# Performance work log

Measured on AMD Instinct MI355X. Metric: run time of the kernel, lower is better.

Reference implementation:

```python
import jax, jax.numpy as jnp
import numpy as np

ROPE_THETA = 10000.0

def _apply_rope(t):
    # t: [B, H, S, D]; rotate interleaved even/odd pairs
    B, H, S, D = t.shape
    inv_freq = 1.0 / (ROPE_THETA ** (jnp.arange(0, D, 2, dtype=jnp.float32) / D))  # [D/2]
    ang = jnp.arange(S, dtype=jnp.float32)[:, None] * inv_freq[None, :]            # [S, D/2]
    cos = jnp.cos(ang)[None, None]  # [1,1,S,D/2]
    sin = jnp.sin(ang)[None, None]
    te = t[..., 0::2]
    to = t[..., 1::2]
    re = te * cos - to * sin
    ro = te * sin + to * cos
    out = jnp.stack([re, ro], axis=-1).reshape(B, H, S, D)
    return out

def setup_inputs() -> dict:
    key = jax.random.key(0)
    ks = jax.random.split(key, 5)
    B, S, DIM = 2, 2048, 2048
    x = jax.random.normal(ks[0], (B, S, DIM), dtype=jnp.float32)
    scale = 0.02
    Wq = jax.random.normal(ks[1], (DIM, DIM), dtype=jnp.float32) * scale
    Wk = jax.random.normal(ks[2], (DIM, DIM), dtype=jnp.float32) * scale
    Wv = jax.random.normal(ks[3], (DIM, DIM), dtype=jnp.float32) * scale
    Wo = jax.random.normal(ks[4], (DIM, DIM), dtype=jnp.float32) * scale
    return {"x": x, "Wq": Wq, "Wk": Wk, "Wv": Wv, "Wo": Wo}

def reference(x, Wq, Wk, Wv, Wo):
    B, S, DIM = x.shape
    H = 16
    HD = DIM // H
    # nn.Linear(bias=False) with weight [out,in]: y = x @ W.T; here W stored [in,out]
    q = (x @ Wq).reshape(B, S, H, HD).transpose(0, 2, 1, 3)  # [B,H,S,HD]
    k = (x @ Wk).reshape(B, S, H, HD).transpose(0, 2, 1, 3)
    v = (x @ Wv).reshape(B, S, H, HD).transpose(0, 2, 1, 3)
    q = _apply_rope(q)
    k = _apply_rope(k)
    scores = jnp.einsum('bhqd,bhkd->bhqk', q, k) / jnp.sqrt(jnp.float32(HD))  # [B,H,S,S]
    causal = jnp.tril(jnp.ones((S, S), dtype=bool))
    scores = jnp.where(causal[None, None], scores, jnp.float32(-jnp.inf))
    attn = jax.nn.softmax(scores, axis=-1)
    out = jnp.einsum('bhqk,bhkd->bhqd', attn, v)            # [B,H,S,HD]
    out = out.transpose(0, 2, 1, 3).reshape(B, S, DIM)
    return out @ Wo  # output projection (dropout is identity in eval)
```

## Files before the change

kernel.cpp:

```cpp
#include <hip/hip_runtime.h>
#include <hip/hip_bf16.h>
#include <math.h>

typedef __bf16 bf16;
typedef __attribute__((ext_vector_type(2))) __bf16 bf16x2;
typedef __attribute__((ext_vector_type(4))) __bf16 bf16x4;
typedef __attribute__((ext_vector_type(8))) __bf16 bf16x8;
typedef __attribute__((ext_vector_type(4))) float f32x4;

#define LDS_ASYNC16(gptr, lptr)                                                        \
  __builtin_amdgcn_global_load_lds(                                                    \
      (const __attribute__((address_space(1))) void*)(gptr),                           \
      (__attribute__((address_space(3))) void*)(lptr), 16, 0, 0)

constexpr int BATCH = 2, SEQ = 2048, DIM = 2048, NH = 16, HD = 128;
constexpr float QSC = 0.12751744f;
constexpr float FREQC = 0.20762050593046f;

template <int CTRL>
__device__ __forceinline__ float dpp_mov_f(float x) {
  return __int_as_float(__builtin_amdgcn_update_dpp(
      __float_as_int(x), __float_as_int(x), CTRL, 0xf, 0xf, false));
}
__device__ __forceinline__ float rowmax16(float x) {
  x = fmaxf(x, dpp_mov_f<0x121>(x));
  x = fmaxf(x, dpp_mov_f<0x122>(x));
  x = fmaxf(x, dpp_mov_f<0x124>(x));
  x = fmaxf(x, dpp_mov_f<0x128>(x));
  return x;
}
__device__ __forceinline__ float rowsum16(float x) {
  x += dpp_mov_f<0x121>(x);
  x += dpp_mov_f<0x122>(x);
  x += dpp_mov_f<0x124>(x);
  x += dpp_mov_f<0x128>(x);
  return x;
}

__global__ void cvt_f32_to_bf16(const float4* __restrict__ in,
                                bf16x4* __restrict__ out, int n4) {
  int i = blockIdx.x * blockDim.x + threadIdx.x;
  if (i >= n4) return;
  float4 v = in[i];
  bf16x4 o;
  o[0] = (bf16)v.x; o[1] = (bf16)v.y; o[2] = (bf16)v.z; o[3] = (bf16)v.w;
  out[i] = o;
}

__global__ void transpose_w4(const float* __restrict__ W0, const float* __restrict__ W1,
                             const float* __restrict__ W2, const float* __restrict__ W3,
                             bf16* __restrict__ T0, bf16* __restrict__ T3) {
  __shared__ float tile[32][33];
  const int z = blockIdx.z;
  const float* W = (z == 0) ? W0 : (z == 1) ? W1 : (z == 2) ? W2 : W3;
  bf16* WT = (z == 3) ? T3 : (T0 + (size_t)z * DIM * DIM);
  int tx = threadIdx.x, ty = threadIdx.y;
  int bx = blockIdx.x * 32, by = blockIdx.y * 32;
#pragma unroll
  for (int j = 0; j < 32; j += 8)
    tile[ty + j][tx] = W[(size_t)(by + ty + j) * DIM + bx + tx];
  __syncthreads();
#pragma unroll
  for (int j = 0; j < 32; j += 8)
    WT[(size_t)(bx + ty + j) * DIM + by + tx] = (bf16)tile[tx][ty + j];
}

__device__ __forceinline__ int swz_src(int c) {
  return (c & 3) ^ ((c >> 3) & 3);
}
__device__ __forceinline__ int swz_rd(int quad, int ln) {
  return quad ^ ((ln >> 1) & 3);
}

__global__ __launch_bounds__(256) void gemm_qkv(const bf16* __restrict__ A,
                                                const bf16* __restrict__ BT,
                                                bf16* __restrict__ Qb,
                                                bf16* __restrict__ Kb,
                                                bf16* __restrict__ VTo) {
  __shared__ __attribute__((aligned(16))) bf16 As[128 * 32];
  __shared__ __attribute__((aligned(16))) bf16 Bs[128 * 32];
  const int tid = threadIdx.x;
  const int w = tid >> 6, lane = tid & 63;
  const int quad = lane >> 4, ln = lane & 15;
  const int m0 = blockIdx.y * 128, n0 = blockIdx.x * 128;
  const int wm = (w >> 1) * 64, wn = (w & 1) * 64;
  const int rdc = swz_rd(quad, ln) * 8;
  f32x4 acc[4][4] = {};

  for (int k0 = 0; k0 < DIM; k0 += 32) {
#pragma unroll
    for (int i = 0; i < 2; ++i) {
      const int c = i * 256 + tid;
      LDS_ASYNC16(A  + (size_t)(m0 + (c >> 2)) * DIM + k0 + swz_src(c) * 8,
                  As + (size_t)(i * 256 + w * 64) * 8);
      LDS_ASYNC16(BT + (size_t)(n0 + (c >> 2)) * DIM + k0 + swz_src(c) * 8,
                  Bs + (size_t)(i * 256 + w * 64) * 8);
    }
    __syncthreads();
    bf16x8 af[4], bfr[4];
#pragma unroll
    for (int t = 0; t < 4; ++t)
      af[t] = *(const bf16x8*)(As + (wm + t * 16 + ln) * 32 + rdc);
#pragma unroll
    for (int t = 0; t < 4; ++t)
      bfr[t] = *(const bf16x8*)(Bs + (wn + t * 16 + ln) * 32 + rdc);
#pragma unroll
    for (int mt = 0; mt < 4; ++mt)
#pragma unroll
      for (int nt = 0; nt < 4; ++nt)
        acc[mt][nt] = __builtin_amdgcn_mfma_f32_16x16x32_bf16(
            af[mt], bfr[nt], acc[mt][nt], 0, 0, 0);
    __syncthreads();
  }

  const int sel = n0 >> 11;
  if (sel == 2) {
#pragma unroll
    for (int mt = 0; mt < 4; ++mt)
#pragma unroll
      for (int nt = 0; nt < 4; ++nt) {
        int gr = m0 + wm + mt * 16 + quad * 4;
        int fc = (n0 + wn + nt * 16 + ln) & 2047;
        int b = gr >> 11, s0 = gr & (SEQ - 1);
        int h = fc >> 7, d = fc & (HD - 1);
        bf16x4 pk;
#pragma unroll
        for (int r = 0; r < 4; ++r) pk[r] = (bf16)acc[mt][nt][r];
        *(bf16x4*)(VTo + ((size_t)((b * NH + h) * HD + d)) * SEQ + s0) = pk;
      }
  } else {
    bf16* Dst = sel ? Kb : Qb;
    const float osc = sel ? 1.0f : QSC;
#pragma unroll
    for (int nt = 0; nt < 4; ++nt) {
      int gc = n0 + wn + nt * 16 + ln;
      int fc = gc & 2047, d = fc & (HD - 1);
      float freq = exp2f(-(float)(d >> 1) * FREQC);
      bool ev = !(d & 1);
#pragma unroll
      for (int mt = 0; mt < 4; ++mt) {
#pragma unroll
        for (int r = 0; r < 4; ++r) {
          int gr = m0 + wm + mt * 16 + quad * 4 + r;
          int s = gr & (SEQ - 1);
          float ang = (float)s * freq;
          float sn, cs;
          __sincosf(ang, &sn, &cs);
          float own = acc[mt][nt][r];
          float oth = __shfl_xor(own, 1);
          float res = ev ? (own * cs - oth * sn) : (oth * sn + own * cs);
          Dst[(size_t)gr * DIM + fc] = (bf16)(res * osc);
        }
      }
    }
  }
}

template <int MODE>
__global__ __launch_bounds__(256) void gemm_bt(const bf16* __restrict__ A,
                                               const bf16* __restrict__ BT,
                                               void* __restrict__ C) {
  __shared__ __attribute__((aligned(16))) bf16 As[128 * 32];
  __shared__ __attribute__((aligned(16))) bf16 Bs[128 * 32];
  const int tid = threadIdx.x;
  const int w = tid >> 6, lane = tid & 63;
  const int quad = lane >> 4, ln = lane & 15;
  const int m0 = blockIdx.y * 128, n0 = blockIdx.x * 128;
  const int wm = (w >> 1) * 64, wn = (w & 1) * 64;
  const int rdc = swz_rd(quad, ln) * 8;
  f32x4 acc[4][4] = {};

  for (int k0 = 0; k0 < DIM; k0 += 32) {
#pragma unroll
    for (int i = 0; i < 2; ++i) {
      const int c = i * 256 + tid;
      LDS_ASYNC16(A  + (size_t)(m0 + (c >> 2)) * DIM + k0 + swz_src(c) * 8,
                  As + (size_t)(i * 256 + w * 64) * 8);
      LDS_ASYNC16(BT + (size_t)(n0 + (c >> 2)) * DIM + k0 + swz_src(c) * 8,
                  Bs + (size_t)(i * 256 + w * 64) * 8);
    }
    __syncthreads();
    bf16x8 af[4], bfr[4];
#pragma unroll
    for (int t = 0; t < 4; ++t)
      af[t] = *(const bf16x8*)(As + (wm + t * 16 + ln) * 32 + rdc);
#pragma unroll
    for (int t = 0; t < 4; ++t)
      bfr[t] = *(const bf16x8*)(Bs + (wn + t * 16 + ln) * 32 + rdc);
#pragma unroll
    for (int mt = 0; mt < 4; ++mt)
#pragma unroll
      for (int nt = 0; nt < 4; ++nt)
        acc[mt][nt] = __builtin_amdgcn_mfma_f32_16x16x32_bf16(
            af[mt], bfr[nt], acc[mt][nt], 0, 0, 0);
    __syncthreads();
  }

  if (MODE == 0) {
    bf16* Co = (bf16*)C;
#pragma unroll
    for (int mt = 0; mt < 4; ++mt)
#pragma unroll
      for (int nt = 0; nt < 4; ++nt) {
        int gr = m0 + wm + mt * 16 + quad * 4;
        int gc = n0 + wn + nt * 16 + ln;
#pragma unroll
        for (int r = 0; r < 4; ++r)
          Co[(size_t)(gr + r) * DIM + gc] = (bf16)acc[mt][nt][r];
      }
  } else {
    float* Co = (float*)C;
#pragma unroll
    for (int mt = 0; mt < 4; ++mt)
#pragma unroll
      for (int nt = 0; nt < 4; ++nt) {
        int gr = m0 + wm + mt * 16 + quad * 4;
        int gc = n0 + wn + nt * 16 + ln;
#pragma unroll
        for (int r = 0; r < 4; ++r)
          Co[(size_t)(gr + r) * DIM + gc] = acc[mt][nt][r];
      }
  }
}

constexpr int PSTR = 72;
__global__ __launch_bounds__(256, 3) void flash_attn(
    const bf16* __restrict__ Q, const bf16* __restrict__ K,
    const bf16* __restrict__ VT, bf16* __restrict__ O,
    bf16* __restrict__ Opart, float* __restrict__ Mpart,
    float* __restrict__ Lpart) {
  __shared__ __attribute__((aligned(16))) bf16 Ks[64 * 128];
  __shared__ __attribute__((aligned(16))) bf16 VTs[128 * 64];
  __shared__ __attribute__((aligned(16))) bf16 Ps[4][32 * PSTR];
  const int tid = threadIdx.x;
  const int w = tid >> 6, lane = tid & 63, quad = lane >> 4, ln = lane & 15;
  const int e = blockIdx.x;
  const int t = (e < 8) ? e : (8 + ((e - 8) >> 1));
  const int c0 = (e < 8) ? 0 : ((e - 8) & 1);
  const bool partial = (e >= 8);
  const int q0 = t * 128;
  const int ktN = 2 * (t + 1);
  const int kt0 = c0 * 16;
  const int kt1 = partial ? ((c0 == 0) ? 16 : ktN) : ktN;
  const int b = blockIdx.y >> 4, h = blockIdx.y & 15;

  bf16x8 qf[2][4];
#pragma unroll
  for (int mt = 0; mt < 2; ++mt)
#pragma unroll
    for (int kc = 0; kc < 4; ++kc)
      qf[mt][kc] = *(const bf16x8*)(Q + ((size_t)b * SEQ + q0 + w * 32 + mt * 16 + ln) * DIM +
                                    h * HD + kc * 32 + quad * 8);
  f32x4 o[2][8] = {};
  float mst[2][4], lst[2][4];
#pragma unroll
  for (int mt = 0; mt < 2; ++mt)
#pragma unroll
    for (int r = 0; r < 4; ++r) { mst[mt][r] = -1e30f; lst[mt][r] = 0.f; }

  for (int kt = kt0; kt < kt1; ++kt) {
    __syncthreads();
#pragma unroll
    for (int i = 0; i < 4; ++i) {
      const int c = i * 256 + tid;
      LDS_ASYNC16(K + ((size_t)b * SEQ + kt * 64 + (c >> 4)) * DIM + h * HD +
                      (((c & 15) ^ ((c >> 4) & 15)) * 8),
                  Ks + (size_t)(i * 256 + w * 64) * 8);
      LDS_ASYNC16(VT + ((size_t)((b * NH + h) * HD) + (c >> 3)) * SEQ + kt * 64 +
                      (((c & 7) ^ ((c >> 3) & 7)) * 8),
                  VTs + (size_t)(i * 256 + w * 64) * 8);
    }
    __syncthreads();

    f32x4 s[2][4] = {};
#pragma unroll
    for (int nt = 0; nt < 4; ++nt) {
      bf16x8 kf[4];
#pragma unroll
      for (int kc = 0; kc < 4; ++kc)
        kf[kc] = *(const bf16x8*)(Ks + (nt * 16 + ln) * 128 +
                                  (((kc * 4 + quad) ^ ln) * 8));
#pragma unroll
      for (int kc = 0; kc < 4; ++kc)
#pragma unroll
        for (int mt = 0; mt < 2; ++mt)
          s[mt][nt] = __builtin_amdgcn_mfma_f32_16x16x32_bf16(
              qf[mt][kc], kf[kc], s[mt][nt], 0, 0, 0);
    }

    const bool diag = (kt * 64 + 63 > q0);
    if (diag) {
#pragma unroll
      for (int mt = 0; mt < 2; ++mt)
#pragma unroll
        for (int nt = 0; nt < 4; ++nt)
#pragma unroll
          for (int r = 0; r < 4; ++r) {
            int kg = kt * 64 + nt * 16 + ln;
            int qg = q0 + w * 32 + mt * 16 + quad * 4 + r;
            if (kg > qg) s[mt][nt][r] = -1e30f;
          }
    }

#pragma unroll
    for (int mt = 0; mt < 2; ++mt)
#pragma unroll
      for (int r = 0; r < 4; ++r) {
        float rm = fmaxf(fmaxf(s[mt][0][r], s[mt][1][r]),
                         fmaxf(s[mt][2][r], s[mt][3][r]));
        rm = rowmax16(rm);
        float mold = mst[mt][r];
        float mnew = fmaxf(mold, rm);
        float alpha = exp2f(mold - mnew);
        mst[mt][r] = mnew;
        float rs = 0.f;
#pragma unroll
        for (int nt = 0; nt < 4; ++nt) {
          float p = exp2f(s[mt][nt][r] - mnew);
          rs += p;
          Ps[w][(mt * 16 + quad * 4 + r) * PSTR + nt * 16 + ln] = (bf16)p;
        }
        lst[mt][r] = lst[mt][r] * alpha + rs;
#pragma unroll
        for (int nd = 0; nd < 8; ++nd) o[mt][nd][r] *= alpha;
      }
    __syncthreads();

#pragma unroll
    for (int kc2 = 0; kc2 < 2; ++kc2) {
      bf16x8 pf[2];
#pragma unroll
      for (int mt = 0; mt < 2; ++mt)
        pf[mt] = *(const bf16x8*)(&Ps[w][(mt * 16 + ln) * PSTR + kc2 * 32 + quad * 8]);
#pragma unroll
      for (int nd = 0; nd < 8; ++nd) {
        bf16x8 vf = *(const bf16x8*)(VTs + (nd * 16 + ln) * 64 +
                                     (((kc2 * 4 + quad) ^ (ln & 7)) * 8));
#pragma unroll
        for (int mt = 0; mt < 2; ++mt)
          o[mt][nd] = __builtin_amdgcn_mfma_f32_16x16x32_bf16(
              pf[mt], vf, o[mt][nd], 0, 0, 0);
      }
    }
  }

  if (!partial) {
#pragma unroll
    for (int mt = 0; mt < 2; ++mt)
#pragma unroll
      for (int r = 0; r < 4; ++r) {
        float inv = 1.f / rowsum16(lst[mt][r]);
        int qg = q0 + w * 32 + mt * 16 + quad * 4 + r;
#pragma unroll
        for (int nd = 0; nd < 8; ++nd)
          O[((size_t)b * SEQ + qg) * DIM + h * HD + nd * 16 + ln] =
              (bf16)(o[mt][nd][r] * inv);
      }
  } else {
    const int slot = (((blockIdx.y << 3) + (t - 8)) << 1) + c0;
    bf16* Op = Opart + (size_t)slot * (128 * 128);
#pragma unroll
    for (int mt = 0; mt < 2; ++mt)
#pragma unroll
      for (int r = 0; r < 4; ++r) {
        float l = rowsum16(lst[mt][r]);
        int qr = w * 32 + mt * 16 + quad * 4 + r;
        if (ln == 0) {
          Mpart[slot * 128 + qr] = mst[mt][r];
          Lpart[slot * 128 + qr] = l;
        }
#pragma unroll
        for (int nd = 0; nd < 8; ++nd)
          Op[qr * 128 + nd * 16 + ln] = (bf16)o[mt][nd][r];
      }
  }
}

__global__ __launch_bounds__(256) void flash_merge(const bf16* __restrict__ Opart,
                                                   const float* __restrict__ Mpart,
                                                   const float* __restrict__ Lpart,
                                                   bf16* __restrict__ O) {
  const int g = blockIdx.x;
  const int bh = g >> 3, t = 8 + (g & 7);
  const int b = bh >> 4, h = bh & 15;
  const int row = threadIdx.x >> 1, half = threadIdx.x & 1;
  const int s0 = g * 2, s1 = g * 2 + 1;
  float m0 = Mpart[s0 * 128 + row], m1 = Mpart[s1 * 128 + row];
  float l0 = Lpart[s0 * 128 + row], l1 = Lpart[s1 * 128 + row];
  float M = fmaxf(m0, m1);
  float w0 = exp2f(m0 - M), w1 = exp2f(m1 - M);
  float inv = 1.f / (w0 * l0 + w1 * l1);
  w0 *= inv; w1 *= inv;
  const bf16* p0 = Opart + (size_t)s0 * (128 * 128) + row * 128 + half * 64;
  const bf16* p1 = Opart + (size_t)s1 * (128 * 128) + row * 128 + half * 64;
  bf16* dst = O + ((size_t)b * SEQ + t * 128 + row) * DIM + h * HD + half * 64;
#pragma unroll
  for (int j = 0; j < 8; ++j) {
    bf16x8 a = *(const bf16x8*)(p0 + j * 8);
    bf16x8 c = *(const bf16x8*)(p1 + j * 8);
    bf16x8 o8;
#pragma unroll
    for (int k = 0; k < 8; ++k)
      o8[k] = (bf16)(w0 * (float)a[k] + w1 * (float)c[k]);
    *(bf16x8*)(dst + j * 8) = o8;
  }
}

extern "C" void kernel_launch(void* const* d_in, const int* in_sizes, int n_in,
                              void* d_out, int out_size, void* d_ws, size_t ws_size,
                              hipStream_t stream) {
  (void)in_sizes; (void)n_in; (void)out_size; (void)ws_size;
  const float* x  = (const float*)d_in[0];
  const float* Wq = (const float*)d_in[1];
  const float* Wk = (const float*)d_in[2];
  const float* Wv = (const float*)d_in[3];
  const float* Wo = (const float*)d_in[4];

  char* ws = (char*)d_ws;
  const size_t MB = 1u << 20;
  const size_t WB = (size_t)DIM * DIM * 2;
  bf16* WTqkv = (bf16*)(ws);
  bf16* WoT   = (bf16*)(ws + 3 * WB);
  bf16* xb    = (bf16*)(ws + 32 * MB);
  bf16* Qb    = (bf16*)(ws + 48 * MB);
  bf16* Kb    = (bf16*)(ws + 64 * MB);
  bf16* VT    = (bf16*)(ws + 80 * MB);
  bf16* Ab    = xb;
  bf16*  Opart = (bf16*)(ws);
  float* Mpart = (float*)(ws + 16 * MB);
  float* Lpart = (float*)(ws + 16 * MB + 256 * 1024);

  int n4 = BATCH * SEQ * DIM / 4;
  cvt_f32_to_bf16<<<n4 / 256, 256, 0, stream>>>((const float4*)x, (bf16x4*)xb, n4);
  dim3 tb(32, 8), tg(DIM / 32, DIM / 32, 4);
  transpose_w4<<<tg, tb, 0, stream>>>(Wq, Wk, Wv, Wo, WTqkv, WoT);

  dim3 qg(3 * DIM / 128, BATCH * SEQ / 128);
  gemm_qkv<<<qg, 256, 0, stream>>>(xb, WTqkv, Qb, Kb, VT);

  dim3 fg(24, BATCH * NH);
  flash_attn<<<fg, 256, 0, stream>>>(Qb, Kb, VT, Ab, Opart, Mpart, Lpart);
  flash_merge<<<256, 256, 0, stream>>>(Opart, Mpart, Lpart, Ab);

  dim3 gg(DIM / 128, BATCH * SEQ / 128);
  gemm_bt<2><<<gg, 256, 0, stream>>>(Ab, WoT, d_out);
}
```

Measured before the change: 469.4 us.

## Double GEMM K-tile to 64 with XOR swizzle and rebalance flash-attention split-K chunks

Both bf16 GEMMs now stage 64-wide K tiles in LDS with an 8-way XOR swizzle, so each barrier pair covers two MFMA k-steps. This halves the number of syncs and load rounds per GEMM, at the cost of twice the LDS per block. Flash attention now splits causal query tiles into chunks of at most 10 key tiles (1 to 4 chunks per tile, 34 blocks per head) instead of a fixed split of the last 8 tiles. The first chunk writes straight into the output buffer, and the merge kernel combines up to 4 partials in place. This aims to balance work across blocks and reduce the tail, in exchange for more partial traffic and more complex indexing.

```diff
diff --git a/kernel.cpp b/kernel.cpp
--- a/kernel.cpp
+++ b/kernel.cpp
@@ -65,51 +65,51 @@
     WT[(size_t)(bx + ty + j) * DIM + by + tx] = (bf16)tile[tx][ty + j];
 }
 
-__device__ __forceinline__ int swz_src(int c) {
-  return (c & 3) ^ ((c >> 3) & 3);
-}
-__device__ __forceinline__ int swz_rd(int quad, int ln) {
-  return quad ^ ((ln >> 1) & 3);
-}
 
 __global__ __launch_bounds__(256) void gemm_qkv(const bf16* __restrict__ A,
                                                 const bf16* __restrict__ BT,
                                                 bf16* __restrict__ Qb,
                                                 bf16* __restrict__ Kb,
                                                 bf16* __restrict__ VTo) {
-  __shared__ __attribute__((aligned(16))) bf16 As[128 * 32];
-  __shared__ __attribute__((aligned(16))) bf16 Bs[128 * 32];
+  __shared__ __attribute__((aligned(16))) bf16 As[128 * 64];
+  __shared__ __attribute__((aligned(16))) bf16 Bs[128 * 64];
   const int tid = threadIdx.x;
   const int w = tid >> 6, lane = tid & 63;
   const int quad = lane >> 4, ln = lane & 15;
   const int m0 = blockIdx.y * 128, n0 = blockIdx.x * 128;
   const int wm = (w >> 1) * 64, wn = (w & 1) * 64;
-  const int rdc = swz_rd(quad, ln) * 8;
+  const int l7 = ln & 7;
   f32x4 acc[4][4] = {};
 
-  for (int k0 = 0; k0 < DIM; k0 += 32) {
-#pragma unroll
-    for (int i = 0; i < 2; ++i) {
+  for (int k0 = 0; k0 < DIM; k0 += 64) {
+#pragma unroll
+    for (int i = 0; i < 4; ++i) {
       const int c = i * 256 + tid;
-      LDS_ASYNC16(A  + (size_t)(m0 + (c >> 2)) * DIM + k0 + swz_src(c) * 8,
+      const int row = c >> 3, p = c & 7;
+      LDS_ASYNC16(A  + (size_t)(m0 + row) * DIM + k0 + ((p ^ (row & 7)) * 8),
                   As + (size_t)(i * 256 + w * 64) * 8);
-      LDS_ASYNC16(BT + (size_t)(n0 + (c >> 2)) * DIM + k0 + swz_src(c) * 8,
+      LDS_ASYNC16(BT + (size_t)(n0 + row) * DIM + k0 + ((p ^ (row & 7)) * 8),
                   Bs + (size_t)(i * 256 + w * 64) * 8);
     }
     __syncthreads();
-    bf16x8 af[4], bfr[4];
-#pragma unroll
-    for (int t = 0; t < 4; ++t)
-      af[t] = *(const bf16x8*)(As + (wm + t * 16 + ln) * 32 + rdc);
-#pragma unroll
-    for (int t = 0; t < 4; ++t)
-      bfr[t] = *(const bf16x8*)(Bs + (wn + t * 16 + ln) * 32 + rdc);
-#pragma unroll
-    for (int mt = 0; mt < 4; ++mt)
-#pragma unroll
-      for (int nt = 0; nt < 4; ++nt)
-        acc[mt][nt] = __builtin_amdgcn_mfma_f32_16x16x32_bf16(
-            af[mt], bfr[nt], acc[mt][nt], 0, 0, 0);
+#pragma unroll
+    for (int kh = 0; kh < 2; ++kh) {
+      bf16x8 af[4], bfr[4];
+#pragma unroll
+      for (int t = 0; t < 4; ++t)
+        af[t] = *(const bf16x8*)(As + (wm + t * 16 + ln) * 64 +
+                                 (((kh * 4 + quad) ^ l7) * 8));
+#pragma unroll
+      for (int t = 0; t < 4; ++t)
+        bfr[t] = *(const bf16x8*)(Bs + (wn + t * 16 + ln) * 64 +
+                                  (((kh * 4 + quad) ^ l7) * 8));
+#pragma unroll
+      for (int mt = 0; mt < 4; ++mt)
+#pragma unroll
+        for (int nt = 0; nt < 4; ++nt)
+          acc[mt][nt] = __builtin_amdgcn_mfma_f32_16x16x32_bf16(
+              af[mt], bfr[nt], acc[mt][nt], 0, 0, 0);
+    }
     __syncthreads();
   }
 
@@ -160,39 +160,45 @@
 __global__ __launch_bounds__(256) void gemm_bt(const bf16* __restrict__ A,
                                                const bf16* __restrict__ BT,
                                                void* __restrict__ C) {
-  __shared__ __attribute__((aligned(16))) bf16 As[128 * 32];
-  __shared__ __attribute__((aligned(16))) bf16 Bs[128 * 32];
+  __shared__ __attribute__((aligned(16))) bf16 As[128 * 64];
+  __shared__ __attribute__((aligned(16))) bf16 Bs[128 * 64];
   const int tid = threadIdx.x;
   const int w = tid >> 6, lane = tid & 63;
   const int quad = lane >> 4, ln = lane & 15;
   const int m0 = blockIdx.y * 128, n0 = blockIdx.x * 128;
   const int wm = (w >> 1) * 64, wn = (w & 1) * 64;
-  const int rdc = swz_rd(quad, ln) * 8;
+  const int l7 = ln & 7;
   f32x4 acc[4][4] = {};
 
-  for (int k0 = 0; k0 < DIM; k0 += 32) {
-#pragma unroll
-    for (int i = 0; i < 2; ++i) {
+  for (int k0 = 0; k0 < DIM; k0 += 64) {
+#pragma unroll
+    for (int i = 0; i < 4; ++i) {
       const int c = i * 256 + tid;
-      LDS_ASYNC16(A  + (size_t)(m0 + (c >> 2)) * DIM + k0 + swz_src(c) * 8,
+      const int row = c >> 3, p = c & 7;
+      LDS_ASYNC16(A  + (size_t)(m0 + row) * DIM + k0 + ((p ^ (row & 7)) * 8),
                   As + (size_t)(i * 256 + w * 64) * 8);
-      LDS_ASYNC16(BT + (size_t)(n0 + (c >> 2)) * DIM + k0 + swz_src(c) * 8,
+      LDS_ASYNC16(BT + (size_t)(n0 + row) * DIM + k0 + ((p ^ (row & 7)) * 8),
                   Bs + (size_t)(i * 256 + w * 64) * 8);
     }
     __syncthreads();
-    bf16x8 af[4], bfr[4];
-#pragma unroll
-    for (int t = 0; t < 4; ++t)
-      af[t] = *(const bf16x8*)(As + (wm + t * 16 + ln) * 32 + rdc);
-#pragma unroll
-    for (int t = 0; t < 4; ++t)
-      bfr[t] = *(const bf16x8*)(Bs + (wn + t * 16 + ln) * 32 + rdc);
-#pragma unroll
-    for (int mt = 0; mt < 4; ++mt)
-#pragma unroll
-      for (int nt = 0; nt < 4; ++nt)
-        acc[mt][nt] = __builtin_amdgcn_mfma_f32_16x16x32_bf16(
-            af[mt], bfr[nt], acc[mt][nt], 0, 0, 0);
+#pragma unroll
+    for (int kh = 0; kh < 2; ++kh) {
+      bf16x8 af[4], bfr[4];
+#pragma unroll
+      for (int t = 0; t < 4; ++t)
+        af[t] = *(const bf16x8*)(As + (wm + t * 16 + ln) * 64 +
+                                 (((kh * 4 + quad) ^ l7) * 8));
+#pragma unroll
+      for (int t = 0; t < 4; ++t)
+        bfr[t] = *(const bf16x8*)(Bs + (wn + t * 16 + ln) * 64 +
+                                  (((kh * 4 + quad) ^ l7) * 8));
+#pragma unroll
+      for (int mt = 0; mt < 4; ++mt)
+#pragma unroll
+        for (int nt = 0; nt < 4; ++nt)
+          acc[mt][nt] = __builtin_amdgcn_mfma_f32_16x16x32_bf16(
+              af[mt], bfr[nt], acc[mt][nt], 0, 0, 0);
+    }
     __syncthreads();
   }
 
@@ -221,6 +227,13 @@
           Co[(size_t)(gr + r) * DIM + gc] = acc[mt][nt][r];
       }
   }
+}
+
+__device__ __forceinline__ int ml_off(int t) {
+  return (t < 10) ? 2 * (t - 5) : (t < 15) ? 10 + 3 * (t - 10) : 25;
+}
+__device__ __forceinline__ int op_off(int t) {
+  return (t < 10) ? (t - 5) : (t < 15) ? 5 + 2 * (t - 10) : 15;
 }
 
 constexpr int PSTR = 72;
@@ -235,14 +248,18 @@
   const int tid = threadIdx.x;
   const int w = tid >> 6, lane = tid & 63, quad = lane >> 4, ln = lane & 15;
   const int e = blockIdx.x;
-  const int t = (e < 8) ? e : (8 + ((e - 8) >> 1));
-  const int c0 = (e < 8) ? 0 : ((e - 8) & 1);
-  const bool partial = (e >= 8);
+  int t, c0, nc;
+  if (e < 5)       { t = e;                  c0 = 0;               nc = 1; }
+  else if (e < 15) { t = 5 + ((e - 5) >> 1); c0 = (e - 5) & 1;     nc = 2; }
+  else if (e < 30) { int q = (e - 15) / 3;   t = 10 + q; c0 = (e - 15) - 3 * q; nc = 3; }
+  else             { t = 15;                 c0 = e - 30;          nc = 4; }
   const int q0 = t * 128;
   const int ktN = 2 * (t + 1);
-  const int kt0 = c0 * 16;
-  const int kt1 = partial ? ((c0 == 0) ? 16 : ktN) : ktN;
-  const int b = blockIdx.y >> 4, h = blockIdx.y & 15;
+  const int kt0 = c0 * 10;
+  const int kt1 = min(kt0 + 10, ktN);
+  const bool chunked = (nc > 1);
+  const int bh = blockIdx.y;
+  const int b = bh >> 4, h = bh & 15;
 
   bf16x8 qf[2][4];
 #pragma unroll
@@ -344,7 +361,7 @@
     }
   }
 
-  if (!partial) {
+  if (!chunked) {
 #pragma unroll
     for (int mt = 0; mt < 2; ++mt)
 #pragma unroll
@@ -357,8 +374,9 @@
               (bf16)(o[mt][nd][r] * inv);
       }
   } else {
-    const int slot = (((blockIdx.y << 3) + (t - 8)) << 1) + c0;
-    bf16* Op = Opart + (size_t)slot * (128 * 128);
+    const int mls = bh * 29 + ml_off(t) + c0;
+    bf16* Op = (c0 == 0) ? nullptr
+                         : Opart + (size_t)(bh * 18 + op_off(t) + (c0 - 1)) * (128 * 128);
 #pragma unroll
     for (int mt = 0; mt < 2; ++mt)
 #pragma unroll
@@ -366,12 +384,19 @@
         float l = rowsum16(lst[mt][r]);
         int qr = w * 32 + mt * 16 + quad * 4 + r;
         if (ln == 0) {
-          Mpart[slot * 128 + qr] = mst[mt][r];
-          Lpart[slot * 128 + qr] = l;
+          Mpart[mls * 128 + qr] = mst[mt][r];
+          Lpart[mls * 128 + qr] = l;
         }
-#pragma unroll
-        for (int nd = 0; nd < 8; ++nd)
-          Op[qr * 128 + nd * 16 + ln] = (bf16)o[mt][nd][r];
+        if (c0 == 0) {
+#pragma unroll
+          for (int nd = 0; nd < 8; ++nd)
+            O[((size_t)b * SEQ + q0 + qr) * DIM + h * HD + nd * 16 + ln] =
+                (bf16)o[mt][nd][r];
+        } else {
+#pragma unroll
+          for (int nd = 0; nd < 8; ++nd)
+            Op[qr * 128 + nd * 16 + ln] = (bf16)o[mt][nd][r];
+        }
       }
   }
 }
@@ -380,28 +405,38 @@
                                                    const float* __restrict__ Mpart,
                                                    const float* __restrict__ Lpart,
                                                    bf16* __restrict__ O) {
-  const int g = blockIdx.x;
-  const int bh = g >> 3, t = 8 + (g & 7);
+  const int bh = blockIdx.x;
+  const int t = 5 + blockIdx.y;
+  const int nc = (t < 10) ? 2 : (t < 15) ? 3 : 4;
   const int b = bh >> 4, h = bh & 15;
   const int row = threadIdx.x >> 1, half = threadIdx.x & 1;
-  const int s0 = g * 2, s1 = g * 2 + 1;
-  float m0 = Mpart[s0 * 128 + row], m1 = Mpart[s1 * 128 + row];
-  float l0 = Lpart[s0 * 128 + row], l1 = Lpart[s1 * 128 + row];
-  float M = fmaxf(m0, m1);
-  float w0 = exp2f(m0 - M), w1 = exp2f(m1 - M);
-  float inv = 1.f / (w0 * l0 + w1 * l1);
-  w0 *= inv; w1 *= inv;
-  const bf16* p0 = Opart + (size_t)s0 * (128 * 128) + row * 128 + half * 64;
-  const bf16* p1 = Opart + (size_t)s1 * (128 * 128) + row * 128 + half * 64;
+  const int mlb = bh * 29 + ml_off(t);
+  float m[4], l[4], wt[4];
+  float M = -1e30f;
+  for (int c = 0; c < nc; ++c) {
+    m[c] = Mpart[(mlb + c) * 128 + row];
+    l[c] = Lpart[(mlb + c) * 128 + row];
+    M = fmaxf(M, m[c]);
+  }
+  float wsum = 0.f;
+  for (int c = 0; c < nc; ++c) { wt[c] = exp2f(m[c] - M); wsum += wt[c] * l[c]; }
+  const float inv = 1.f / wsum;
   bf16* dst = O + ((size_t)b * SEQ + t * 128 + row) * DIM + h * HD + half * 64;
+  const bf16* pb = Opart + (size_t)(bh * 18 + op_off(t)) * (128 * 128) + row * 128 + half * 64;
 #pragma unroll
   for (int j = 0; j < 8; ++j) {
-    bf16x8 a = *(const bf16x8*)(p0 + j * 8);
-    bf16x8 c = *(const bf16x8*)(p1 + j * 8);
+    bf16x8 a0 = *(const bf16x8*)(dst + j * 8);
+    float acc[8];
+#pragma unroll
+    for (int k = 0; k < 8; ++k) acc[k] = wt[0] * (float)a0[k];
+    for (int c = 1; c < nc; ++c) {
+      bf16x8 a = *(const bf16x8*)(pb + (size_t)(c - 1) * (128 * 128) + j * 8);
+#pragma unroll
+      for (int k = 0; k < 8; ++k) acc[k] += wt[c] * (float)a[k];
+    }
     bf16x8 o8;
 #pragma unroll
-    for (int k = 0; k < 8; ++k)
-      o8[k] = (bf16)(w0 * (float)a[k] + w1 * (float)c[k]);
+    for (int k = 0; k < 8; ++k) o8[k] = (bf16)(acc[k] * inv);
     *(bf16x8*)(dst + j * 8) = o8;
   }
 }
@@ -427,8 +462,8 @@
   bf16* VT    = (bf16*)(ws + 80 * MB);
   bf16* Ab    = xb;
   bf16*  Opart = (bf16*)(ws);
-  float* Mpart = (float*)(ws + 16 * MB);
-  float* Lpart = (float*)(ws + 16 * MB + 256 * 1024);
+  float* Mpart = (float*)(ws + 19 * MB);
+  float* Lpart = (float*)(ws + 19 * MB + 512 * 1024);
 
   int n4 = BATCH * SEQ * DIM / 4;
   cvt_f32_to_bf16<<<n4 / 256, 256, 0, stream>>>((const float4*)x, (bf16x4*)xb, n4);
@@ -438,9 +473,10 @@
   dim3 qg(3 * DIM / 128, BATCH * SEQ / 128);
   gemm_qkv<<<qg, 256, 0, stream>>>(xb, WTqkv, Qb, Kb, VT);
 
-  dim3 fg(24, BATCH * NH);
+  dim3 fg(34, BATCH * NH);
   flash_attn<<<fg, 256, 0, stream>>>(Qb, Kb, VT, Ab, Opart, Mpart, Lpart);
-  flash_merge<<<256, 256, 0, stream>>>(Opart, Mpart, Lpart, Ab);
+  dim3 mg(BATCH * NH, 11);
+  flash_merge<<<mg, 256, 0, stream>>>(Opart, Mpart, Lpart, Ab);
 
   dim3 gg(DIM / 128, BATCH * SEQ / 128);
   gemm_bt<2><<<gg, 256, 0, stream>>>(Ab, WoT, d_out);
```

Result: no change. 461.7 us (-1.6%).
